# Optimization experiments

Hardware: AMD Instinct MI355X
Metric: run time of the kernel (lower is better)

Reference implementation:

```python
import jax, jax.numpy as jnp
import numpy as np

FE = 16
L = 32 * FE            # 512 input spatial size
K5 = 5 + 8 * (FE - 1)  # 125, C5 kernel so output is 1x1
F6_OUT = 16 * 24 * FE * FE  # 98304

# LeNet-5 sparse connection table for C3, read off the slicing in ConvC3.forward
C3_GROUPS = [
    [0, 1, 2], [1, 2, 3], [2, 3, 4], [3, 4, 5], [4, 5, 0], [5, 0, 1],
    [0, 1, 2, 3], [1, 2, 3, 4], [2, 3, 4, 5], [3, 4, 5, 0], [4, 5, 0, 1], [5, 0, 1, 2],
    [0, 1, 3, 4], [1, 2, 4, 5], [0, 2, 3, 5], [0, 1, 2, 3, 4, 5],
]

def c3_mask():
    m = np.zeros((16, 6, 1, 1), np.float32)
    for o, g in enumerate(C3_GROUPS):
        m[o, g, 0, 0] = 1.0
    return jnp.asarray(m)

_C3_MASK = c3_mask()

def conv2d(x, w, b):
    # x: (C,H,W) unbatched; w: (O,I,kh,kw); VALID, stride 1
    y = jax.lax.conv_general_dilated(x[None], w, (1, 1), 'VALID',
                                     dimension_numbers=('NCHW', 'OIHW', 'NCHW'))[0]
    return y + b[:, None, None]

def avgpool2(x):
    C, H, W = x.shape
    return x.reshape(C, H // 2, 2, W // 2, 2).mean(axis=(2, 4))

def setup_inputs() -> dict:
    key = jax.random.key(0)
    ks = jax.random.split(key, 6)
    x = jax.random.normal(ks[0], (1, L, L), dtype=jnp.float32)
    W1 = jax.random.normal(ks[1], (6, 1, 5, 5), dtype=jnp.float32) * 0.1
    b1 = jnp.zeros((6,), jnp.float32)
    W3 = jax.random.normal(ks[2], (16, 6, 5, 5), dtype=jnp.float32) * 0.1
    b3 = jnp.zeros((16,), jnp.float32)
    W5 = jax.random.normal(ks[3], (120, 16, K5, K5), dtype=jnp.float32) * 0.01
    b5 = jnp.zeros((120,), jnp.float32)
    W6 = jax.random.normal(ks[4], (F6_OUT, 120), dtype=jnp.float32) * 0.05
    b6 = jnp.zeros((F6_OUT,), jnp.float32)
    W7 = jax.random.normal(ks[5], (54, F6_OUT), dtype=jnp.float32) * 0.01
    b7 = jnp.zeros((54,), jnp.float32)
    return {"x": x, "W1": W1, "b1": b1, "W3": W3, "b3": b3,
            "W5": W5, "b5": b5, "W6": W6, "b6": b6, "W7": W7, "b7": b7}

def reference(x, W1, b1, W3, b3, W5, b5, W6, b6, W7, b7):
    relu = jax.nn.relu
    h = relu(conv2d(x, W1, b1))            # (6, 508, 508)
    h = avgpool2(h)                        # (6, 254, 254)
    # C3: 16 tiny sparse-connected 5x5 convs fused into one masked dense conv
    h = relu(conv2d(h, W3 * _C3_MASK, b3)) # (16, 250, 250)
    h = avgpool2(h)                        # (16, 125, 125)
    h = relu(conv2d(h, W5, b5))            # (120, 1, 1)
    h = h.reshape(-1, 120)                 # (1, 120)
    h = relu(h @ W6.T + b6)                # (1, 98304)
    return h @ W7.T + b7                   # (1, 54)
```

## Files before the change

kernel.cpp:

```cpp
#include <hip/hip_runtime.h>

typedef float f32x4 __attribute__((ext_vector_type(4)));

#define P1 254
#define P2 125
#define C5_K 250000
#define C5_K4 62500
#define C5_CHUNK_F4 5000
#undef C5_CHUNK_F4
#define C5_CHUNK_F4 3125
#define F6_OUT 98304
#define F7_K4 24576
#define F7_CHUNK_F4 2048

#define WS_H2 0
#define WS_H4 400000
#define WS_C5 650000
#define WS_H6 650128

__device__ __forceinline__ float4 nt_load4(const float4* p) {
    f32x4 v = __builtin_nontemporal_load((const f32x4*)p);
    return make_float4(v.x, v.y, v.z, v.w);
}

__global__ __launch_bounds__(256) void c1_s2_kernel(const float* __restrict__ x,
        const float* __restrict__ W1, const float* __restrict__ b1,
        float* __restrict__ h2,
        const float* __restrict__ b5, const float* __restrict__ b7,
        float* __restrict__ c5acc, float* __restrict__ out) {
    if (blockIdx.x == 0) {
        int t = threadIdx.x;
        if (t < 120) c5acc[t] = b5[t];
        if (t >= 128 && t < 182) out[t - 128] = b7[t - 128];
    }
    int t = blockIdx.x * 256 + threadIdx.x;
    const int total = 6 * P1 * P1;
    if (t >= total) return;
    int c  = t / (P1 * P1);
    int r  = t % (P1 * P1);
    int y  = r / P1, x0 = r % P1;

    float w[25];
    #pragma unroll
    for (int k = 0; k < 25; ++k) w[k] = W1[c * 25 + k];

    float p[6][6];
    const float2* xin2 = (const float2*)(x + (2 * y) * 512 + 2 * x0);
    #pragma unroll
    for (int i = 0; i < 6; ++i) {
        float2 a0 = xin2[i * 256 + 0];
        float2 a1 = xin2[i * 256 + 1];
        float2 a2 = xin2[i * 256 + 2];
        p[i][0] = a0.x; p[i][1] = a0.y; p[i][2] = a1.x;
        p[i][3] = a1.y; p[i][4] = a2.x; p[i][5] = a2.y;
    }

    float bias = b1[c];
    float s = 0.f;
    #pragma unroll
    for (int dy = 0; dy < 2; ++dy)
        #pragma unroll
        for (int dx = 0; dx < 2; ++dx) {
            float a = bias;
            #pragma unroll
            for (int kh = 0; kh < 5; ++kh)
                #pragma unroll
                for (int kw = 0; kw < 5; ++kw)
                    a = fmaf(p[dy + kh][dx + kw], w[kh * 5 + kw], a);
            s += fmaxf(a, 0.f);
        }
    h2[t] = 0.25f * s;
}

__global__ __launch_bounds__(256) void c3_s4_kernel(const float* __restrict__ h2,
        const float* __restrict__ W3, const float* __restrict__ b3,
        float* __restrict__ h4) {
    const unsigned char MASK[16] = {7,14,28,56,49,35,15,30,60,57,51,39,27,54,45,63};
    int t = blockIdx.x * 256 + threadIdx.x;
    const int total = 16 * P2 * P2;
    if (t >= total) return;
    int o  = t / (P2 * P2);
    int r  = t % (P2 * P2);
    int y  = r / P2, x0 = r % P2;

    float a00, a01, a10, a11;
    a00 = a01 = a10 = a11 = b3[o];
    unsigned m = MASK[o];

    for (int i = 0; i < 6; ++i) {
        if (!((m >> i) & 1)) continue;
        const float2* hp2 = (const float2*)(h2 + i * P1 * P1 + (2 * y) * P1 + 2 * x0);
        const float* wp = W3 + (o * 6 + i) * 25;
        float w[25];
        #pragma unroll
        for (int k = 0; k < 25; ++k) w[k] = wp[k];
        float p[6][6];
        #pragma unroll
        for (int ii = 0; ii < 6; ++ii) {
            float2 a0 = hp2[ii * 127 + 0];
            float2 a1 = hp2[ii * 127 + 1];
            float2 a2 = hp2[ii * 127 + 2];
            p[ii][0] = a0.x; p[ii][1] = a0.y; p[ii][2] = a1.x;
            p[ii][3] = a1.y; p[ii][4] = a2.x; p[ii][5] = a2.y;
        }
        #pragma unroll
        for (int kh = 0; kh < 5; ++kh)
            #pragma unroll
            for (int kw = 0; kw < 5; ++kw) {
                float wv = w[kh * 5 + kw];
                a00 = fmaf(p[kh][kw],         wv, a00);
                a01 = fmaf(p[kh][kw + 1],     wv, a01);
                a10 = fmaf(p[kh + 1][kw],     wv, a10);
                a11 = fmaf(p[kh + 1][kw + 1], wv, a11);
            }
    }
    h4[t] = 0.25f * (fmaxf(a00, 0.f) + fmaxf(a01, 0.f) + fmaxf(a10, 0.f) + fmaxf(a11, 0.f));
}

__device__ __forceinline__ float block_reduce_256(float v) {
    #pragma unroll
    for (int off = 32; off > 0; off >>= 1) v += __shfl_down(v, off, 64);
    __shared__ float s[4];
    int lane = threadIdx.x & 63, wv = threadIdx.x >> 6;
    if (lane == 0) s[wv] = v;
    __syncthreads();
    return s[0] + s[1] + s[2] + s[3];
}

__global__ __launch_bounds__(256) void c5_kernel(const float* __restrict__ h4,
        const float* __restrict__ W5, float* __restrict__ c5acc) {
    int row = blockIdx.y;
    const float4* wr = (const float4*)(W5 + (size_t)row * C5_K);
    const float4* hv = (const float4*)h4;
    int start = blockIdx.x * C5_CHUNK_F4;
    int end   = start + C5_CHUNK_F4;
    float s = 0.f;
    for (int i = start + (int)threadIdx.x; i < end; i += 256) {
        float4 w = nt_load4(&wr[i]);
        float4 h = hv[i];
        s = fmaf(w.x, h.x, s); s = fmaf(w.y, h.y, s);
        s = fmaf(w.z, h.z, s); s = fmaf(w.w, h.w, s);
    }
    s = block_reduce_256(s);
    if (threadIdx.x == 0) atomicAdd(&c5acc[row], s);
}

#define F6_RPB 128
#define F6_STRIDE 124
__global__ __launch_bounds__(256) void f6_kernel(const float* __restrict__ c5acc,
        const float* __restrict__ W6, const float* __restrict__ b6,
        float* __restrict__ h6) {
    __shared__ float ws6[F6_RPB * F6_STRIDE];
    __shared__ float h5s[120];
    int tid = threadIdx.x;
    int base = blockIdx.x * F6_RPB;
    if (tid < 120) h5s[tid] = fmaxf(c5acc[tid], 0.f);
    const float4* src = (const float4*)(W6 + (size_t)base * 120);
    #pragma unroll
    for (int i = 0; i < 15; ++i) {
        int f4 = tid + i * 256;
        float4 v = nt_load4(&src[f4]);
        int flat = f4 * 4;
        int row = flat / 120;
        int col = flat - row * 120;
        *(float4*)&ws6[row * F6_STRIDE + col] = v;
    }
    __syncthreads();
    int row  = tid >> 1;
    int half = tid & 1;
    const float4* wr4 = (const float4*)&ws6[row * F6_STRIDE + half * 60];
    const float4* hh4 = (const float4*)&h5s[half * 60];
    float a = 0.f;
    #pragma unroll
    for (int j = 0; j < 15; ++j) {
        float4 w = wr4[j], h = hh4[j];
        a = fmaf(w.x, h.x, a); a = fmaf(w.y, h.y, a);
        a = fmaf(w.z, h.z, a); a = fmaf(w.w, h.w, a);
    }
    a += __shfl_xor(a, 1, 64);
    if (half == 0) {
        int o = base + row;
        h6[o] = fmaxf(a + b6[o], 0.f);
    }
}

__global__ __launch_bounds__(256) void f7_kernel(const float* __restrict__ h6,
        const float* __restrict__ W7, float* __restrict__ out) {
    int row = blockIdx.y;
    const float4* wr = (const float4*)(W7 + (size_t)row * (F7_K4 * 4));
    const float4* hv = (const float4*)h6;
    int start = blockIdx.x * F7_CHUNK_F4;
    int end   = start + F7_CHUNK_F4;
    float s = 0.f;
    for (int i = start + (int)threadIdx.x; i < end; i += 256) {
        float4 w = nt_load4(&wr[i]);
        float4 h = hv[i];
        s = fmaf(w.x, h.x, s); s = fmaf(w.y, h.y, s);
        s = fmaf(w.z, h.z, s); s = fmaf(w.w, h.w, s);
    }
    s = block_reduce_256(s);
    if (threadIdx.x == 0) atomicAdd(&out[row], s);
}

extern "C" void kernel_launch(void* const* d_in, const int* in_sizes, int n_in,
                              void* d_out, int out_size, void* d_ws, size_t ws_size,
                              hipStream_t stream) {
    const float* x  = (const float*)d_in[0];
    const float* W1 = (const float*)d_in[1];
    const float* b1 = (const float*)d_in[2];
    const float* W3 = (const float*)d_in[3];
    const float* b3 = (const float*)d_in[4];
    const float* W5 = (const float*)d_in[5];
    const float* b5 = (const float*)d_in[6];
    const float* W6 = (const float*)d_in[7];
    const float* b6 = (const float*)d_in[8];
    const float* W7 = (const float*)d_in[9];
    const float* b7 = (const float*)d_in[10];
    float* out = (float*)d_out;
    float* ws  = (float*)d_ws;

    float* h2 = ws + WS_H2;
    float* h4 = ws + WS_H4;
    float* c5 = ws + WS_C5;
    float* h6 = ws + WS_H6;

    {
        int total = 6 * P1 * P1;
        c1_s2_kernel<<<(total + 255) / 256, 256, 0, stream>>>(x, W1, b1, h2, b5, b7, c5, out);
    }
    {
        int total = 16 * P2 * P2;
        c3_s4_kernel<<<(total + 255) / 256, 256, 0, stream>>>(h2, W3, b3, h4);
    }
    c5_kernel<<<dim3(C5_K4 / C5_CHUNK_F4, 120), 256, 0, stream>>>(h4, W5, c5);
    f6_kernel<<<F6_OUT / F6_RPB, 256, 0, stream>>>(c5, W6, b6, h6);
    f7_kernel<<<dim3(F7_K4 / F7_CHUNK_F4, 54), 256, 0, stream>>>(h6, W7, out);
}
```

Measured before the change: 273.2 us.

## Fuse F6 and F7 into one kernel with per-block partial F7 atomics

Merges the F6 and F7 layers into a single kernel. Each block computes its 128 F6 outputs into shared memory, then immediately multiplies them against the matching 128-column slice of W7 and atomically adds partials into the 54 outputs. This removes one launch and the global round trip of the 98304-element hidden vector. The cost is many more atomics (768 blocks × 54) and W7 reads done as strided 512-byte row segments rather than long contiguous streams.

```diff
diff --git a/kernel.cpp b/kernel.cpp
--- a/kernel.cpp
+++ b/kernel.cpp
@@ -6,17 +6,12 @@
 #define P2 125
 #define C5_K 250000
 #define C5_K4 62500
-#define C5_CHUNK_F4 5000
-#undef C5_CHUNK_F4
 #define C5_CHUNK_F4 3125
 #define F6_OUT 98304
-#define F7_K4 24576
-#define F7_CHUNK_F4 2048
 
 #define WS_H2 0
 #define WS_H4 400000
 #define WS_C5 650000
-#define WS_H6 650128
 
 __device__ __forceinline__ float4 nt_load4(const float4* p) {
     f32x4 v = __builtin_nontemporal_load((const f32x4*)p);
@@ -147,11 +142,12 @@
 
 #define F6_RPB 128
 #define F6_STRIDE 124
-__global__ __launch_bounds__(256) void f6_kernel(const float* __restrict__ c5acc,
+__global__ __launch_bounds__(256) void f6f7_kernel(const float* __restrict__ c5acc,
         const float* __restrict__ W6, const float* __restrict__ b6,
-        float* __restrict__ h6) {
+        const float* __restrict__ W7, float* __restrict__ out) {
     __shared__ float ws6[F6_RPB * F6_STRIDE];
     __shared__ float h5s[120];
+    __shared__ float h6s[F6_RPB];
     int tid = threadIdx.x;
     int base = blockIdx.x * F6_RPB;
     if (tid < 120) h5s[tid] = fmaxf(c5acc[tid], 0.f);
@@ -166,40 +162,36 @@
         *(float4*)&ws6[row * F6_STRIDE + col] = v;
     }
     __syncthreads();
-    int row  = tid >> 1;
-    int half = tid & 1;
-    const float4* wr4 = (const float4*)&ws6[row * F6_STRIDE + half * 60];
-    const float4* hh4 = (const float4*)&h5s[half * 60];
-    float a = 0.f;
-    #pragma unroll
-    for (int j = 0; j < 15; ++j) {
-        float4 w = wr4[j], h = hh4[j];
-        a = fmaf(w.x, h.x, a); a = fmaf(w.y, h.y, a);
-        a = fmaf(w.z, h.z, a); a = fmaf(w.w, h.w, a);
-    }
-    a += __shfl_xor(a, 1, 64);
-    if (half == 0) {
-        int o = base + row;
-        h6[o] = fmaxf(a + b6[o], 0.f);
-    }
-}
-
-__global__ __launch_bounds__(256) void f7_kernel(const float* __restrict__ h6,
-        const float* __restrict__ W7, float* __restrict__ out) {
-    int row = blockIdx.y;
-    const float4* wr = (const float4*)(W7 + (size_t)row * (F7_K4 * 4));
-    const float4* hv = (const float4*)h6;
-    int start = blockIdx.x * F7_CHUNK_F4;
-    int end   = start + F7_CHUNK_F4;
-    float s = 0.f;
-    for (int i = start + (int)threadIdx.x; i < end; i += 256) {
-        float4 w = nt_load4(&wr[i]);
-        float4 h = hv[i];
-        s = fmaf(w.x, h.x, s); s = fmaf(w.y, h.y, s);
-        s = fmaf(w.z, h.z, s); s = fmaf(w.w, h.w, s);
-    }
-    s = block_reduce_256(s);
-    if (threadIdx.x == 0) atomicAdd(&out[row], s);
+    {
+        int row  = tid >> 1;
+        int half = tid & 1;
+        const float4* wr4 = (const float4*)&ws6[row * F6_STRIDE + half * 60];
+        const float4* hh4 = (const float4*)&h5s[half * 60];
+        float a = 0.f;
+        #pragma unroll
+        for (int j = 0; j < 15; ++j) {
+            float4 w = wr4[j], h = hh4[j];
+            a = fmaf(w.x, h.x, a); a = fmaf(w.y, h.y, a);
+            a = fmaf(w.z, h.z, a); a = fmaf(w.w, h.w, a);
+        }
+        a += __shfl_xor(a, 1, 64);
+        if (half == 0) h6s[row] = fmaxf(a + b6[base + row], 0.f);
+    }
+    __syncthreads();
+    {
+        int wv = tid >> 6, lane = tid & 63;
+        float h0 = h6s[lane], h1 = h6s[lane + 64];
+        for (int o = wv; o < 54; o += 4) {
+            const float* w7r = W7 + (size_t)o * F6_OUT + base;
+            float2 wv2;
+            wv2.x = __builtin_nontemporal_load(w7r + lane);
+            wv2.y = __builtin_nontemporal_load(w7r + lane + 64);
+            float p = fmaf(wv2.x, h0, wv2.y * h1);
+            #pragma unroll
+            for (int off = 32; off > 0; off >>= 1) p += __shfl_down(p, off, 64);
+            if (lane == 0) atomicAdd(&out[o], p);
+        }
+    }
 }
 
 extern "C" void kernel_launch(void* const* d_in, const int* in_sizes, int n_in,
@@ -222,7 +214,6 @@
     float* h2 = ws + WS_H2;
     float* h4 = ws + WS_H4;
     float* c5 = ws + WS_C5;
-    float* h6 = ws + WS_H6;
 
     {
         int total = 6 * P1 * P1;
@@ -233,6 +224,5 @@
         c3_s4_kernel<<<(total + 255) / 256, 256, 0, stream>>>(h2, W3, b3, h4);
     }
     c5_kernel<<<dim3(C5_K4 / C5_CHUNK_F4, 120), 256, 0, stream>>>(h4, W5, c5);
-    f6_kernel<<<F6_OUT / F6_RPB, 256, 0, stream>>>(c5, W6, b6, h6);
-    f7_kernel<<<dim3(F7_K4 / F7_CHUNK_F4, 54), 256, 0, stream>>>(h6, W7, out);
-}
+    f6f7_kernel<<<F6_OUT / F6_RPB, 256, 0, stream>>>(c5, W6, b6, W7, out);
+}
```

Result: slower. 557.5 us (+104.1%).
